# Kernel optimization log

Hardware: AMD Instinct MI355X
Metric: run time of the kernel (lower is better)

Reference implementation:

```python
import jax, jax.numpy as jnp
import numpy as np

N = 50000       # nodes
E = 800000      # edges (before self-loops)
B = 1024        # graphs
D = 256         # emb = hidden = representation size
OUT = 128
NFEAT = 9       # OGB atom features
VOCAB = 100
NLAYERS = 4     # 1 + hidden_layers(2) + 1
NEG_SLOPE = 0.2


def setup_inputs() -> dict:
    key = jax.random.key(0)
    ks = jax.random.split(key, 10)
    x = jax.random.randint(ks[0], (N, NFEAT), 0, VOCAB)
    edge_index = jax.random.randint(ks[1], (2, E), 0, N)
    batch = jnp.sort(jax.random.randint(ks[2], (N,), 0, B))
    atom_emb = jax.random.normal(ks[3], (NFEAT, VOCAB, D), jnp.float32) * 0.1
    Ws = jax.random.normal(ks[4], (NLAYERS, D, D), jnp.float32) * (1.0 / np.sqrt(D))
    a_src = jax.random.normal(ks[5], (NLAYERS, D), jnp.float32) * 0.1
    a_dst = jax.random.normal(ks[6], (NLAYERS, D), jnp.float32) * 0.1
    biases = jnp.zeros((NLAYERS, D), jnp.float32)
    lin_w = jax.random.normal(ks[7], (3 * D, OUT), jnp.float32) * (1.0 / np.sqrt(3 * D))
    lin_b = jnp.zeros((OUT,), jnp.float32)
    return dict(x=x, edge_index=edge_index, batch=batch, atom_emb=atom_emb,
                Ws=Ws, a_src=a_src, a_dst=a_dst, biases=biases,
                lin_w=lin_w, lin_b=lin_b)


def _gat_layer(h, src, dst, W, asrc, adst, b):
    # PyG GATConv, heads=1: linear transform, per-edge additive attention,
    # segment softmax over incoming edges of each target, scatter-add aggregate.
    h = h @ W                                        # [N, D]
    s = jnp.einsum('nd,d->n', h, asrc)               # source-side score
    t = jnp.einsum('nd,d->n', h, adst)               # target-side score
    e = jax.nn.leaky_relu(s[src] + t[dst], NEG_SLOPE)  # [E']
    m = jax.ops.segment_max(e, dst, num_segments=N)  # segment softmax (stable)
    e = jnp.exp(e - m[dst])
    denom = jax.ops.segment_sum(e, dst, num_segments=N)
    alpha = e / denom[dst]                           # self-loops ensure denom > 0
    out = jax.ops.segment_sum(alpha[:, None] * h[src], dst, num_segments=N)
    return out + b


def reference(x, edge_index, batch, atom_emb, Ws, a_src, a_dst, biases, lin_w, lin_b):
    # AtomEncoder: sum of per-feature embedding lookups -> [N, D]
    h = atom_emb[jnp.arange(NFEAT)[:, None], x.T].sum(axis=0)
    # add self-loops once (GATConv default add_self_loops=True)
    loops = jnp.arange(N)
    src = jnp.concatenate([edge_index[0], loops])
    dst = jnp.concatenate([edge_index[1], loops])
    for l in range(NLAYERS):
        h = _gat_layer(h, src, dst, Ws[l], a_src[l], a_dst[l], biases[l])
        h = jax.nn.relu(h)
    # global mean / add / max pooling over graphs
    count = jax.ops.segment_sum(jnp.ones((N,), h.dtype), batch, num_segments=B)
    x_add = jax.ops.segment_sum(h, batch, num_segments=B)
    x_mean = x_add / jnp.maximum(count, 1.0)[:, None]
    x_max = jax.ops.segment_max(h, batch, num_segments=B)
    x_max = jnp.where(count[:, None] > 0, x_max, 0.0)
    feats = jnp.concatenate([x_mean, x_add, x_max], axis=1)  # [B, 3D]
    # dropout is identity in eval mode
    return feats @ lin_w + lin_b
```

## Files before the change

### kernel.cpp

```cpp
#include <hip/hip_runtime.h>
#include <math.h>

#define N_NODES 50000
#define N_EDGES 800000
#define NGRAPH  1024
#define D       256
#define OUTD    128
#define NFEAT   9
#define VOCABSZ 100
#define NLAYERS 4
#define NEG_SLOPE 0.2f
#define SCAN_NBLK ((N_NODES + 255) / 256)

typedef __attribute__((ext_vector_type(8))) short short8;
typedef __attribute__((ext_vector_type(4))) float f32x4;

static __device__ __forceinline__ unsigned short f2bf(float f) {
    unsigned int u = __float_as_uint(f);
    u = (u + 0x7FFFu + ((u >> 16) & 1u)) >> 16;
    return (unsigned short)u;
}
static __device__ __forceinline__ float bf2f(unsigned short u) {
    return __uint_as_float(((unsigned int)u) << 16);
}

#define GLOAD_LDS16(g, l) __builtin_amdgcn_global_load_lds( \
    (const __attribute__((address_space(1))) void*)(g), \
    (__attribute__((address_space(3))) void*)(l), 16, 0, 0)

__global__ void set_deg_one(int* deg) {
    int v = blockIdx.x * blockDim.x + threadIdx.x;
    if (v < N_NODES) deg[v] = 1;
}

__global__ void hist_dst(const int* __restrict__ dst, int* __restrict__ deg) {
    int e = blockIdx.x * blockDim.x + threadIdx.x;
    if (e < N_EDGES) atomicAdd(&deg[dst[e]], 1);
}

__global__ __launch_bounds__(256) void block_sum(const int* __restrict__ deg, int* __restrict__ bsum) {
    int i = blockIdx.x * 256 + threadIdx.x;
    int v = (i < N_NODES) ? deg[i] : 0;
    #pragma unroll
    for (int off = 32; off; off >>= 1) v += __shfl_down(v, off, 64);
    __shared__ int ws[4];
    if ((threadIdx.x & 63) == 0) ws[threadIdx.x >> 6] = v;
    __syncthreads();
    if (threadIdx.x == 0) bsum[blockIdx.x] = ws[0] + ws[1] + ws[2] + ws[3];
}

__global__ __launch_bounds__(256) void scan_bsum(int* __restrict__ bsum, int* __restrict__ rowptr) {
    __shared__ int sh[256];
    int tid = threadIdx.x;
    int v = (tid < SCAN_NBLK) ? bsum[tid] : 0;
    sh[tid] = v;
    __syncthreads();
    for (int off = 1; off < 256; off <<= 1) {
        int u = (tid >= off) ? sh[tid - off] : 0;
        __syncthreads();
        sh[tid] += u;
        __syncthreads();
    }
    if (tid < SCAN_NBLK) bsum[tid] = (tid > 0) ? sh[tid - 1] : 0;
    if (tid == SCAN_NBLK - 1) rowptr[N_NODES] = sh[tid];
}

__global__ __launch_bounds__(256) void scan_block(const int* __restrict__ deg,
                                                  const int* __restrict__ boffs,
                                                  int* __restrict__ rowptr) {
    __shared__ int sh[256];
    int tid = threadIdx.x;
    int i = blockIdx.x * 256 + tid;
    int v = (i < N_NODES) ? deg[i] : 0;
    sh[tid] = v;
    __syncthreads();
    for (int off = 1; off < 256; off <<= 1) {
        int u = (tid >= off) ? sh[tid - off] : 0;
        __syncthreads();
        sh[tid] += u;
        __syncthreads();
    }
    if (i < N_NODES) rowptr[i] = boffs[blockIdx.x] + sh[tid] - v;
}

__global__ void init_cursor(const int* __restrict__ rowptr, int* __restrict__ cursor, int* __restrict__ ssrc) {
    int v = blockIdx.x * blockDim.x + threadIdx.x;
    if (v < N_NODES) {
        int p = rowptr[v];
        cursor[v] = p + 1;
        ssrc[p] = v;
    }
}

__global__ void scatter_edges(const int* __restrict__ src, const int* __restrict__ dst,
                              int* __restrict__ cursor, int* __restrict__ ssrc) {
    int e = blockIdx.x * blockDim.x + threadIdx.x;
    if (e < N_EDGES) {
        int pos = atomicAdd(&cursor[dst[e]], 1);
        ssrc[pos] = src[e];
    }
}

__global__ __launch_bounds__(256) void wt_kernel(const float* __restrict__ W, unsigned short* __restrict__ Wt) {
    int t = blockIdx.x * 256 + threadIdx.x;
    int l = t >> 16;
    int k = (t >> 8) & 255;
    int n = t & 255;
    float v = W[t];
    Wt[(l << 16) + n * 256 + k] = f2bf(v);
}

__global__ void zero_st(float* __restrict__ s, float* __restrict__ t) {
    int i = blockIdx.x * blockDim.x + threadIdx.x;
    if (i < N_NODES) { s[i] = 0.f; t[i] = 0.f; }
}

__global__ __launch_bounds__(256) void atom_encoder(const int* __restrict__ x,
                                                    const float* __restrict__ emb,
                                                    unsigned short* __restrict__ h) {
    int node = blockIdx.x * 4 + (threadIdx.x >> 6);
    int lane = threadIdx.x & 63;
    if (node >= N_NODES) return;
    float4 acc = make_float4(0.f, 0.f, 0.f, 0.f);
    #pragma unroll
    for (int f = 0; f < NFEAT; ++f) {
        int xi = x[node * NFEAT + f];
        float4 v = *(const float4*)&emb[(size_t)(f * VOCABSZ + xi) * D + lane * 4];
        acc.x += v.x; acc.y += v.y; acc.z += v.z; acc.w += v.w;
    }
    ushort4 o;
    o.x = f2bf(acc.x); o.y = f2bf(acc.y); o.z = f2bf(acc.z); o.w = f2bf(acc.w);
    *(ushort4*)&h[node * D + lane * 4] = o;
}

#define GBM 128
#define GBN 128
#define GBK 64
__global__ __launch_bounds__(256) void gemm_bf16(const unsigned short* __restrict__ A,
                                                 const unsigned short* __restrict__ Wt,
                                                 const float* __restrict__ asrc,
                                                 const float* __restrict__ adst,
                                                 unsigned short* __restrict__ C,
                                                 float* __restrict__ s_out,
                                                 float* __restrict__ t_out) {
    __shared__ unsigned short a_s[2][GBM * GBK];
    __shared__ unsigned short b_s[2][GBM * GBK];
    int row0 = blockIdx.x * GBM;
    int col0 = blockIdx.y * GBN;
    int tid = threadIdx.x;
    int wid = tid >> 6;
    int lane = tid & 63;
    int wm = wid >> 1, wn = wid & 1;
    int l15 = lane & 15;
    int lhi = lane >> 4;

    int srcA[4], srcB[4];
    #pragma unroll
    for (int q = 0; q < 4; ++q) {
        int slot = (wid * 4 + q) * 64 + lane;
        int r = slot >> 3, c = slot & 7;
        int ra = row0 + r; if (ra > N_NODES - 1) ra = N_NODES - 1;
        srcA[q] = ra * D + ((c ^ (r & 7)) << 3);
        srcB[q] = (col0 + r) * D + ((c ^ (r & 7)) << 3);
    }

    f32x4 acc[4][4];
    #pragma unroll
    for (int i = 0; i < 4; ++i)
        #pragma unroll
        for (int j = 0; j < 4; ++j) acc[i][j] = (f32x4){0.f, 0.f, 0.f, 0.f};

    #pragma unroll
    for (int q = 0; q < 4; ++q) {
        GLOAD_LDS16(A + srcA[q], &a_s[0][(wid * 4 + q) * 512]);
        GLOAD_LDS16(Wt + srcB[q], &b_s[0][(wid * 4 + q) * 512]);
    }
    __syncthreads();

    #pragma unroll
    for (int step = 0; step < 4; ++step) {
        int cur = step & 1;
        if (step < 3) {
            int k0 = (step + 1) * GBK;
            #pragma unroll
            for (int q = 0; q < 4; ++q) {
                GLOAD_LDS16(A + srcA[q] + k0, &a_s[cur ^ 1][(wid * 4 + q) * 512]);
                GLOAD_LDS16(Wt + srcB[q] + k0, &b_s[cur ^ 1][(wid * 4 + q) * 512]);
            }
        }
        #pragma unroll
        for (int ks = 0; ks < 2; ++ks) {
            short8 af[4], bf[4];
            #pragma unroll
            for (int m = 0; m < 4; ++m) {
                int r = wm * 64 + m * 16 + l15;
                int c = ks * 4 + lhi;
                af[m] = *(const short8*)&a_s[cur][r * GBK + ((c ^ (r & 7)) << 3)];
            }
            #pragma unroll
            for (int n = 0; n < 4; ++n) {
                int r = wn * 64 + n * 16 + l15;
                int c = ks * 4 + lhi;
                bf[n] = *(const short8*)&b_s[cur][r * GBK + ((c ^ (r & 7)) << 3)];
            }
            #pragma unroll
            for (int m = 0; m < 4; ++m)
                #pragma unroll
                for (int n = 0; n < 4; ++n)
                    acc[m][n] = __builtin_amdgcn_mfma_f32_16x16x32_bf16(af[m], bf[n], acc[m][n], 0, 0, 0);
        }
        __syncthreads();
    }

    #pragma unroll
    for (int m = 0; m < 4; ++m) {
        #pragma unroll
        for (int r = 0; r < 4; ++r) {
            int grow = row0 + wm * 64 + m * 16 + lhi * 4 + r;
            if (grow < N_NODES) {
                #pragma unroll
                for (int n = 0; n < 4; ++n) {
                    int gcol = col0 + wn * 64 + n * 16 + l15;
                    C[(size_t)grow * D + gcol] = f2bf(acc[m][n][r]);
                }
            }
        }
    }

    float av[4], bv[4];
    #pragma unroll
    for (int n = 0; n < 4; ++n) {
        int gcol = col0 + wn * 64 + n * 16 + l15;
        av[n] = asrc[gcol];
        bv[n] = adst[gcol];
    }
    #pragma unroll
    for (int m = 0; m < 4; ++m) {
        #pragma unroll
        for (int r = 0; r < 4; ++r) {
            float ps = 0.f, pt = 0.f;
            #pragma unroll
            for (int n = 0; n < 4; ++n) {
                ps += acc[m][n][r] * av[n];
                pt += acc[m][n][r] * bv[n];
            }
            #pragma unroll
            for (int off = 1; off < 16; off <<= 1) {
                ps += __shfl_xor(ps, off, 64);
                pt += __shfl_xor(pt, off, 64);
            }
            int grow = row0 + wm * 64 + m * 16 + lhi * 4 + r;
            if (l15 == 0 && grow < N_NODES) {
                atomicAdd(&s_out[grow], ps);
                atomicAdd(&t_out[grow], pt);
            }
        }
    }
}

__global__ __launch_bounds__(256) void aggregate_kernel(const unsigned short* __restrict__ hW,
                                                        const float* __restrict__ s,
                                                        const float* __restrict__ t,
                                                        const int* __restrict__ rowptr,
                                                        const int* __restrict__ ssrc,
                                                        const float* __restrict__ bias,
                                                        unsigned short* __restrict__ hout) {
    int v = (blockIdx.x * blockDim.x + threadIdx.x) >> 6;
    int lane = threadIdx.x & 63;
    if (v >= N_NODES) return;
    int beg = rowptr[v];
    int deg = rowptr[v + 1] - beg;
    float tv = t[v];
    float m = -1e30f;
    float denom = 0.f;
    float acc[8];
    #pragma unroll
    for (int j = 0; j < 8; ++j) acc[j] = 0.f;
    int half = lane >> 5;
    int l32 = lane & 31;

    for (int base = 0; base < deg; base += 64) {
        int rem = deg - base; if (rem > 64) rem = 64;
        int u = 0; float e = -1e30f;
        if (lane < rem) {
            u = ssrc[beg + base + lane];
            float ev = s[u] + tv;
            e = (ev > 0.f) ? ev : NEG_SLOPE * ev;
        }
        float cm = e;
        #pragma unroll
        for (int off = 32; off; off >>= 1) cm = fmaxf(cm, __shfl_xor(cm, off, 64));
        float newm = fmaxf(m, cm);
        float scale = __expf(m - newm);
        float p = (lane < rem) ? __expf(e - newm) : 0.f;
        float ws = p;
        #pragma unroll
        for (int off = 32; off; off >>= 1) ws += __shfl_xor(ws, off, 64);
        denom = denom * scale + ws;
        m = newm;
        #pragma unroll
        for (int j = 0; j < 8; ++j) acc[j] *= scale;
        for (int i = 0; i < rem; i += 4) {
            int idx0 = i + half;
            int idx1 = i + 2 + half;
            float p0 = __shfl(p, idx0, 64);
            int   u0 = __shfl(u, idx0, 64);
            float p1 = __shfl(p, idx1, 64);
            int   u1 = __shfl(u, idx1, 64);
            short8 hv0 = *(const short8*)&hW[(size_t)u0 * D + l32 * 8];
            short8 hv1 = *(const short8*)&hW[(size_t)u1 * D + l32 * 8];
            #pragma unroll
            for (int j = 0; j < 8; ++j)
                acc[j] += p0 * bf2f((unsigned short)hv0[j]);
            #pragma unroll
            for (int j = 0; j < 8; ++j)
                acc[j] += p1 * bf2f((unsigned short)hv1[j]);
        }
    }
    #pragma unroll
    for (int j = 0; j < 8; ++j) acc[j] += __shfl_xor(acc[j], 32, 64);
    float inv = 1.f / denom;
    if (half == 0) {
        float4 b0 = *(const float4*)&bias[l32 * 8];
        float4 b1 = *(const float4*)&bias[l32 * 8 + 4];
        float bb[8] = {b0.x, b0.y, b0.z, b0.w, b1.x, b1.y, b1.z, b1.w};
        short8 o;
        #pragma unroll
        for (int j = 0; j < 8; ++j) {
            float val = fmaxf(acc[j] * inv + bb[j], 0.f);
            o[j] = (short)f2bf(val);
        }
        *(short8*)&hout[(size_t)v * D + l32 * 8] = o;
    }
}

__global__ void growptr_kernel(const int* __restrict__ batch, int* __restrict__ growptr) {
    int n = blockIdx.x * blockDim.x + threadIdx.x;
    if (n >= N_NODES) return;
    int b = batch[n];
    int prev = (n == 0) ? -1 : batch[n - 1];
    for (int g = prev + 1; g <= b; ++g) growptr[g] = n;
    if (n == N_NODES - 1) {
        for (int g = b + 1; g <= NGRAPH; ++g) growptr[g] = N_NODES;
    }
}

__global__ __launch_bounds__(256) void pool_kernel(const unsigned short* __restrict__ h,
                                                   const int* __restrict__ growptr,
                                                   float* __restrict__ feats) {
    int g = (blockIdx.x * blockDim.x + threadIdx.x) >> 6;
    int lane = threadIdx.x & 63;
    if (g >= NGRAPH) return;
    int beg = growptr[g], end = growptr[g + 1];
    float4 add = make_float4(0.f, 0.f, 0.f, 0.f);
    float4 mx = make_float4(-1e30f, -1e30f, -1e30f, -1e30f);
    for (int v = beg; v < end; ++v) {
        ushort4 hv = *(const ushort4*)&h[(size_t)v * D + lane * 4];
        float h0 = bf2f(hv.x), h1 = bf2f(hv.y), h2 = bf2f(hv.z), h3 = bf2f(hv.w);
        add.x += h0; add.y += h1; add.z += h2; add.w += h3;
        mx.x = fmaxf(mx.x, h0); mx.y = fmaxf(mx.y, h1);
        mx.z = fmaxf(mx.z, h2); mx.w = fmaxf(mx.w, h3);
    }
    float cnt = (float)(end - beg);
    float invc = 1.f / fmaxf(cnt, 1.f);
    if (cnt <= 0.f) { mx = make_float4(0.f, 0.f, 0.f, 0.f); }
    float4 mean = make_float4(add.x * invc, add.y * invc, add.z * invc, add.w * invc);
    float* fr = feats + (size_t)g * 3 * D;
    *(float4*)&fr[0 * D + 4 * lane] = mean;
    *(float4*)&fr[1 * D + 4 * lane] = add;
    *(float4*)&fr[2 * D + 4 * lane] = mx;
}

__global__ __launch_bounds__(128) void final_linear(const float* __restrict__ feats,
                                                    const float* __restrict__ lw,
                                                    const float* __restrict__ lb,
                                                    float* __restrict__ out) {
    int g = blockIdx.x;
    int j = threadIdx.x;
    __shared__ float f[3 * D];
    for (int i = j; i < 3 * D; i += OUTD) f[i] = feats[(size_t)g * 3 * D + i];
    __syncthreads();
    float acc = lb[j];
    #pragma unroll 8
    for (int k = 0; k < 3 * D; ++k)
        acc += f[k] * lw[k * OUTD + j];
    out[g * OUTD + j] = acc;
}

extern "C" void kernel_launch(void* const* d_in, const int* in_sizes, int n_in,
                              void* d_out, int out_size, void* d_ws, size_t ws_size,
                              hipStream_t stream) {
    const int*   x        = (const int*)d_in[0];
    const int*   edge_idx = (const int*)d_in[1];
    const int*   batch    = (const int*)d_in[2];
    const float* atom_emb = (const float*)d_in[3];
    const float* Ws       = (const float*)d_in[4];
    const float* a_src    = (const float*)d_in[5];
    const float* a_dst    = (const float*)d_in[6];
    const float* biases   = (const float*)d_in[7];
    const float* lin_w    = (const float*)d_in[8];
    const float* lin_b    = (const float*)d_in[9];
    float* out = (float*)d_out;

    char* ws = (char*)d_ws;
    size_t off = 0;
    auto alloc = [&](size_t bytes) -> void* {
        void* p = ws + off;
        off += (bytes + 255) & ~(size_t)255;
        return p;
    };
    unsigned short* bufA = (unsigned short*)alloc(sizeof(short) * (size_t)N_NODES * D);
    unsigned short* bufB = (unsigned short*)alloc(sizeof(short) * (size_t)N_NODES * D);
    unsigned short* Wt   = (unsigned short*)alloc(sizeof(short) * NLAYERS * D * D);
    float* s      = (float*)alloc(sizeof(float) * N_NODES);
    float* t      = (float*)alloc(sizeof(float) * N_NODES);
    int*   deg    = (int*)alloc(sizeof(int) * N_NODES);
    int*   rowptr = (int*)alloc(sizeof(int) * (N_NODES + 1));
    int*   bsum   = (int*)alloc(sizeof(int) * 256);
    int*   ssrc   = (int*)alloc(sizeof(int) * (N_EDGES + N_NODES));
    int*   growp  = (int*)alloc(sizeof(int) * (NGRAPH + 1));
    float* feats  = (float*)alloc(sizeof(float) * (size_t)NGRAPH * 3 * D);

    const int* esrc = edge_idx;
    const int* edst = edge_idx + N_EDGES;

    set_deg_one<<<(N_NODES + 255) / 256, 256, 0, stream>>>(deg);
    hist_dst<<<(N_EDGES + 255) / 256, 256, 0, stream>>>(edst, deg);
    block_sum<<<SCAN_NBLK, 256, 0, stream>>>(deg, bsum);
    scan_bsum<<<1, 256, 0, stream>>>(bsum, rowptr);
    scan_block<<<SCAN_NBLK, 256, 0, stream>>>(deg, bsum, rowptr);
    init_cursor<<<(N_NODES + 255) / 256, 256, 0, stream>>>(rowptr, deg, ssrc);
    scatter_edges<<<(N_EDGES + 255) / 256, 256, 0, stream>>>(esrc, edst, deg, ssrc);

    wt_kernel<<<NLAYERS * D * D / 256, 256, 0, stream>>>(Ws, Wt);
    atom_encoder<<<(N_NODES + 3) / 4, 256, 0, stream>>>(x, atom_emb, bufA);

    for (int l = 0; l < NLAYERS; ++l) {
        zero_st<<<(N_NODES + 255) / 256, 256, 0, stream>>>(s, t);
        dim3 ggrid((N_NODES + GBM - 1) / GBM, D / GBN);
        gemm_bf16<<<ggrid, 256, 0, stream>>>(bufA, Wt + (size_t)l * D * D,
                                             a_src + l * D, a_dst + l * D,
                                             bufB, s, t);
        aggregate_kernel<<<(N_NODES + 3) / 4, 256, 0, stream>>>(bufB, s, t, rowptr, ssrc,
                                                                biases + l * D, bufA);
    }

    growptr_kernel<<<(N_NODES + 255) / 256, 256, 0, stream>>>(batch, growp);
    pool_kernel<<<(NGRAPH + 3) / 4, 256, 0, stream>>>(bufA, growp, feats);
    final_linear<<<NGRAPH, OUTD, 0, stream>>>(feats, lin_w, lin_b, out);
}
```

Measured before the change: 536.2 us.

## Unroll aggregate gathers with packed FMA, unroll pooling, batch graphs in final linear

The aggregation loop now issues four neighbour row gathers per iteration instead of two and accumulates with packed two-wide float math using bit-shift bf16 unpacking. Pooling unrolls the node loop by four to raise memory-level parallelism. The final linear layer processes eight graphs per block, so each weight load is reused eight times. Costs are higher register pressure in aggregate and fewer blocks in the final linear.

```diff
diff --git a/kernel.cpp b/kernel.cpp
--- a/kernel.cpp
+++ b/kernel.cpp
@@ -14,6 +14,7 @@
 
 typedef __attribute__((ext_vector_type(8))) short short8;
 typedef __attribute__((ext_vector_type(4))) float f32x4;
+typedef __attribute__((ext_vector_type(2))) float f32x2;
 
 static __device__ __forceinline__ unsigned short f2bf(float f) {
     unsigned int u = __float_as_uint(f);
@@ -273,11 +274,12 @@
     float tv = t[v];
     float m = -1e30f;
     float denom = 0.f;
-    float acc[8];
-    #pragma unroll
-    for (int j = 0; j < 8; ++j) acc[j] = 0.f;
+    f32x2 acc2[4];
+    #pragma unroll
+    for (int j = 0; j < 4; ++j) acc2[j] = (f32x2){0.f, 0.f};
     int half = lane >> 5;
     int l32 = lane & 31;
+    const unsigned short* hbase = hW + (size_t)l32 * 8;
 
     for (int base = 0; base < deg; base += 64) {
         int rem = deg - base; if (rem > 64) rem = 64;
@@ -299,35 +301,55 @@
         denom = denom * scale + ws;
         m = newm;
         #pragma unroll
-        for (int j = 0; j < 8; ++j) acc[j] *= scale;
-        for (int i = 0; i < rem; i += 4) {
-            int idx0 = i + half;
-            int idx1 = i + 2 + half;
-            float p0 = __shfl(p, idx0, 64);
-            int   u0 = __shfl(u, idx0, 64);
-            float p1 = __shfl(p, idx1, 64);
-            int   u1 = __shfl(u, idx1, 64);
-            short8 hv0 = *(const short8*)&hW[(size_t)u0 * D + l32 * 8];
-            short8 hv1 = *(const short8*)&hW[(size_t)u1 * D + l32 * 8];
-            #pragma unroll
-            for (int j = 0; j < 8; ++j)
-                acc[j] += p0 * bf2f((unsigned short)hv0[j]);
-            #pragma unroll
-            for (int j = 0; j < 8; ++j)
-                acc[j] += p1 * bf2f((unsigned short)hv1[j]);
-        }
-    }
-    #pragma unroll
-    for (int j = 0; j < 8; ++j) acc[j] += __shfl_xor(acc[j], 32, 64);
+        for (int j = 0; j < 4; ++j) acc2[j] *= scale;
+        for (int i = 0; i < rem; i += 8) {
+            float pj[4]; int uj[4];
+            #pragma unroll
+            for (int j = 0; j < 4; ++j) {
+                int idx = i + 2 * j + half;
+                pj[j] = __shfl(p, idx, 64);
+                uj[j] = __shfl(u, idx, 64);
+            }
+            uint4 w[4];
+            #pragma unroll
+            for (int j = 0; j < 4; ++j)
+                w[j] = *(const uint4*)(hbase + ((size_t)uj[j] << 8));
+            #pragma unroll
+            for (int j = 0; j < 4; ++j) {
+                f32x2 p2 = (f32x2){pj[j], pj[j]};
+                unsigned int ww;
+                f32x2 h2;
+                ww = w[j].x;
+                h2 = (f32x2){__uint_as_float(ww << 16), __uint_as_float(ww & 0xffff0000u)};
+                acc2[0] += p2 * h2;
+                ww = w[j].y;
+                h2 = (f32x2){__uint_as_float(ww << 16), __uint_as_float(ww & 0xffff0000u)};
+                acc2[1] += p2 * h2;
+                ww = w[j].z;
+                h2 = (f32x2){__uint_as_float(ww << 16), __uint_as_float(ww & 0xffff0000u)};
+                acc2[2] += p2 * h2;
+                ww = w[j].w;
+                h2 = (f32x2){__uint_as_float(ww << 16), __uint_as_float(ww & 0xffff0000u)};
+                acc2[3] += p2 * h2;
+            }
+        }
+    }
+    #pragma unroll
+    for (int j = 0; j < 4; ++j) {
+        acc2[j].x += __shfl_xor(acc2[j].x, 32, 64);
+        acc2[j].y += __shfl_xor(acc2[j].y, 32, 64);
+    }
     float inv = 1.f / denom;
     if (half == 0) {
         float4 b0 = *(const float4*)&bias[l32 * 8];
         float4 b1 = *(const float4*)&bias[l32 * 8 + 4];
         float bb[8] = {b0.x, b0.y, b0.z, b0.w, b1.x, b1.y, b1.z, b1.w};
+        float av[8] = {acc2[0].x, acc2[0].y, acc2[1].x, acc2[1].y,
+                       acc2[2].x, acc2[2].y, acc2[3].x, acc2[3].y};
         short8 o;
         #pragma unroll
         for (int j = 0; j < 8; ++j) {
-            float val = fmaxf(acc[j] * inv + bb[j], 0.f);
+            float val = fmaxf(av[j] * inv + bb[j], 0.f);
             o[j] = (short)f2bf(val);
         }
         *(short8*)&hout[(size_t)v * D + l32 * 8] = o;
@@ -354,12 +376,27 @@
     int beg = growptr[g], end = growptr[g + 1];
     float4 add = make_float4(0.f, 0.f, 0.f, 0.f);
     float4 mx = make_float4(-1e30f, -1e30f, -1e30f, -1e30f);
-    for (int v = beg; v < end; ++v) {
+    int v = beg;
+    for (; v + 4 <= end; v += 4) {
+        ushort4 h0 = *(const ushort4*)&h[(size_t)(v + 0) * D + lane * 4];
+        ushort4 h1 = *(const ushort4*)&h[(size_t)(v + 1) * D + lane * 4];
+        ushort4 h2 = *(const ushort4*)&h[(size_t)(v + 2) * D + lane * 4];
+        ushort4 h3 = *(const ushort4*)&h[(size_t)(v + 3) * D + lane * 4];
+        ushort4 hs[4] = {h0, h1, h2, h3};
+        #pragma unroll
+        for (int q = 0; q < 4; ++q) {
+            float a0 = bf2f(hs[q].x), a1 = bf2f(hs[q].y), a2 = bf2f(hs[q].z), a3 = bf2f(hs[q].w);
+            add.x += a0; add.y += a1; add.z += a2; add.w += a3;
+            mx.x = fmaxf(mx.x, a0); mx.y = fmaxf(mx.y, a1);
+            mx.z = fmaxf(mx.z, a2); mx.w = fmaxf(mx.w, a3);
+        }
+    }
+    for (; v < end; ++v) {
         ushort4 hv = *(const ushort4*)&h[(size_t)v * D + lane * 4];
-        float h0 = bf2f(hv.x), h1 = bf2f(hv.y), h2 = bf2f(hv.z), h3 = bf2f(hv.w);
-        add.x += h0; add.y += h1; add.z += h2; add.w += h3;
-        mx.x = fmaxf(mx.x, h0); mx.y = fmaxf(mx.y, h1);
-        mx.z = fmaxf(mx.z, h2); mx.w = fmaxf(mx.w, h3);
+        float a0 = bf2f(hv.x), a1 = bf2f(hv.y), a2 = bf2f(hv.z), a3 = bf2f(hv.w);
+        add.x += a0; add.y += a1; add.z += a2; add.w += a3;
+        mx.x = fmaxf(mx.x, a0); mx.y = fmaxf(mx.y, a1);
+        mx.z = fmaxf(mx.z, a2); mx.w = fmaxf(mx.w, a3);
     }
     float cnt = (float)(end - beg);
     float invc = 1.f / fmaxf(cnt, 1.f);
@@ -371,20 +408,30 @@
     *(float4*)&fr[2 * D + 4 * lane] = mx;
 }
 
+#define GPB 8
 __global__ __launch_bounds__(128) void final_linear(const float* __restrict__ feats,
                                                     const float* __restrict__ lw,
                                                     const float* __restrict__ lb,
                                                     float* __restrict__ out) {
-    int g = blockIdx.x;
+    int g0 = blockIdx.x * GPB;
     int j = threadIdx.x;
-    __shared__ float f[3 * D];
-    for (int i = j; i < 3 * D; i += OUTD) f[i] = feats[(size_t)g * 3 * D + i];
+    __shared__ float f[GPB][3 * D];
+    for (int i = j; i < GPB * 3 * D; i += OUTD)
+        f[i / (3 * D)][i % (3 * D)] = feats[(size_t)g0 * 3 * D + i];
     __syncthreads();
-    float acc = lb[j];
-    #pragma unroll 8
-    for (int k = 0; k < 3 * D; ++k)
-        acc += f[k] * lw[k * OUTD + j];
-    out[g * OUTD + j] = acc;
+    float acc[GPB];
+    float lbv = lb[j];
+    #pragma unroll
+    for (int g = 0; g < GPB; ++g) acc[g] = lbv;
+    for (int k = 0; k < 3 * D; ++k) {
+        float w = lw[k * OUTD + j];
+        #pragma unroll
+        for (int g = 0; g < GPB; ++g)
+            acc[g] += f[g][k] * w;
+    }
+    #pragma unroll
+    for (int g = 0; g < GPB; ++g)
+        out[(g0 + g) * OUTD + j] = acc[g];
 }
 
 extern "C" void kernel_launch(void* const* d_in, const int* in_sizes, int n_in,
@@ -447,5 +494,5 @@
 
     growptr_kernel<<<(N_NODES + 255) / 256, 256, 0, stream>>>(batch, growp);
     pool_kernel<<<(NGRAPH + 3) / 4, 256, 0, stream>>>(bufA, growp, feats);
-    final_linear<<<NGRAPH, OUTD, 0, stream>>>(feats, lin_w, lin_b, out);
-}
+    final_linear<<<NGRAPH / GPB, OUTD, 0, stream>>>(feats, lin_w, lin_b, out);
+}
```

Result: no change. 537.2 us (+0.2%).

## Stage GEMM output through LDS, batch final linear, hoist s/t zeroing, unroll pooling

Applied to the files above, without the earlier changes.

Four separate changes. The GEMM epilogue now writes the bf16 tile to padded shared memory and then issues coalesced 16-byte row stores, replacing scattered 2-byte stores. The per-layer zero_st launches become one up-front init over per-layer s/t buffers. The final linear processes 8 graphs per block so each weight load is reused. Pooling is unrolled by 4 nodes. The cost is extra LDS traffic and a barrier in the epilogue, plus a little more workspace for the per-layer s/t buffers.

```diff
diff --git a/kernel.cpp b/kernel.cpp
--- a/kernel.cpp
+++ b/kernel.cpp
@@ -28,9 +28,10 @@
     (const __attribute__((address_space(1))) void*)(g), \
     (__attribute__((address_space(3))) void*)(l), 16, 0, 0)
 
-__global__ void set_deg_one(int* deg) {
-    int v = blockIdx.x * blockDim.x + threadIdx.x;
-    if (v < N_NODES) deg[v] = 1;
+__global__ void init_all(int* __restrict__ deg, float* __restrict__ s_all, float* __restrict__ t_all) {
+    int i = blockIdx.x * blockDim.x + threadIdx.x;
+    if (i < N_NODES) deg[i] = 1;
+    if (i < NLAYERS * N_NODES) { s_all[i] = 0.f; t_all[i] = 0.f; }
 }
 
 __global__ void hist_dst(const int* __restrict__ dst, int* __restrict__ deg) {
@@ -108,11 +109,6 @@
     int n = t & 255;
     float v = W[t];
     Wt[(l << 16) + n * 256 + k] = f2bf(v);
-}
-
-__global__ void zero_st(float* __restrict__ s, float* __restrict__ t) {
-    int i = blockIdx.x * blockDim.x + threadIdx.x;
-    if (i < N_NODES) { s[i] = 0.f; t[i] = 0.f; }
 }
 
 __global__ __launch_bounds__(256) void atom_encoder(const int* __restrict__ x,
@@ -143,8 +139,7 @@
                                                  unsigned short* __restrict__ C,
                                                  float* __restrict__ s_out,
                                                  float* __restrict__ t_out) {
-    __shared__ unsigned short a_s[2][GBM * GBK];
-    __shared__ unsigned short b_s[2][GBM * GBK];
+    __shared__ unsigned short smem[32768];
     int row0 = blockIdx.x * GBM;
     int col0 = blockIdx.y * GBN;
     int tid = threadIdx.x;
@@ -172,8 +167,8 @@
 
     #pragma unroll
     for (int q = 0; q < 4; ++q) {
-        GLOAD_LDS16(A + srcA[q], &a_s[0][(wid * 4 + q) * 512]);
-        GLOAD_LDS16(Wt + srcB[q], &b_s[0][(wid * 4 + q) * 512]);
+        GLOAD_LDS16(A + srcA[q], &smem[(wid * 4 + q) * 512]);
+        GLOAD_LDS16(Wt + srcB[q], &smem[16384 + (wid * 4 + q) * 512]);
     }
     __syncthreads();
 
@@ -184,10 +179,12 @@
             int k0 = (step + 1) * GBK;
             #pragma unroll
             for (int q = 0; q < 4; ++q) {
-                GLOAD_LDS16(A + srcA[q] + k0, &a_s[cur ^ 1][(wid * 4 + q) * 512]);
-                GLOAD_LDS16(Wt + srcB[q] + k0, &b_s[cur ^ 1][(wid * 4 + q) * 512]);
-            }
-        }
+                GLOAD_LDS16(A + srcA[q] + k0, &smem[(cur ^ 1) * 8192 + (wid * 4 + q) * 512]);
+                GLOAD_LDS16(Wt + srcB[q] + k0, &smem[16384 + (cur ^ 1) * 8192 + (wid * 4 + q) * 512]);
+            }
+        }
+        const unsigned short* aS = &smem[cur * 8192];
+        const unsigned short* bS = &smem[16384 + cur * 8192];
         #pragma unroll
         for (int ks = 0; ks < 2; ++ks) {
             short8 af[4], bf[4];
@@ -195,13 +192,13 @@
             for (int m = 0; m < 4; ++m) {
                 int r = wm * 64 + m * 16 + l15;
                 int c = ks * 4 + lhi;
-                af[m] = *(const short8*)&a_s[cur][r * GBK + ((c ^ (r & 7)) << 3)];
+                af[m] = *(const short8*)&aS[r * GBK + ((c ^ (r & 7)) << 3)];
             }
             #pragma unroll
             for (int n = 0; n < 4; ++n) {
                 int r = wn * 64 + n * 16 + l15;
                 int c = ks * 4 + lhi;
-                bf[n] = *(const short8*)&b_s[cur][r * GBK + ((c ^ (r & 7)) << 3)];
+                bf[n] = *(const short8*)&bS[r * GBK + ((c ^ (r & 7)) << 3)];
             }
             #pragma unroll
             for (int m = 0; m < 4; ++m)
@@ -212,18 +209,29 @@
         __syncthreads();
     }
 
+    unsigned short* c_s = smem;
     #pragma unroll
     for (int m = 0; m < 4; ++m) {
         #pragma unroll
         for (int r = 0; r < 4; ++r) {
-            int grow = row0 + wm * 64 + m * 16 + lhi * 4 + r;
-            if (grow < N_NODES) {
-                #pragma unroll
-                for (int n = 0; n < 4; ++n) {
-                    int gcol = col0 + wn * 64 + n * 16 + l15;
-                    C[(size_t)grow * D + gcol] = f2bf(acc[m][n][r]);
-                }
-            }
+            int lr = wm * 64 + m * 16 + lhi * 4 + r;
+            #pragma unroll
+            for (int n = 0; n < 4; ++n) {
+                int lc = wn * 64 + n * 16 + l15;
+                c_s[lr * 132 + lc] = f2bf(acc[m][n][r]);
+            }
+        }
+    }
+    __syncthreads();
+    #pragma unroll
+    for (int p = 0; p < 8; ++p) {
+        int slot = p * 256 + tid;
+        int r2 = slot >> 4;
+        int c2 = slot & 15;
+        int grow = row0 + r2;
+        if (grow < N_NODES) {
+            short8 vv = *(const short8*)&c_s[r2 * 132 + c2 * 8];
+            *(short8*)&C[(size_t)grow * D + col0 + c2 * 8] = vv;
         }
     }
 
@@ -354,12 +362,27 @@
     int beg = growptr[g], end = growptr[g + 1];
     float4 add = make_float4(0.f, 0.f, 0.f, 0.f);
     float4 mx = make_float4(-1e30f, -1e30f, -1e30f, -1e30f);
-    for (int v = beg; v < end; ++v) {
+    int v = beg;
+    for (; v + 4 <= end; v += 4) {
+        ushort4 h0 = *(const ushort4*)&h[(size_t)(v + 0) * D + lane * 4];
+        ushort4 h1 = *(const ushort4*)&h[(size_t)(v + 1) * D + lane * 4];
+        ushort4 h2 = *(const ushort4*)&h[(size_t)(v + 2) * D + lane * 4];
+        ushort4 h3 = *(const ushort4*)&h[(size_t)(v + 3) * D + lane * 4];
+        ushort4 hs[4] = {h0, h1, h2, h3};
+        #pragma unroll
+        for (int q = 0; q < 4; ++q) {
+            float a0 = bf2f(hs[q].x), a1 = bf2f(hs[q].y), a2 = bf2f(hs[q].z), a3 = bf2f(hs[q].w);
+            add.x += a0; add.y += a1; add.z += a2; add.w += a3;
+            mx.x = fmaxf(mx.x, a0); mx.y = fmaxf(mx.y, a1);
+            mx.z = fmaxf(mx.z, a2); mx.w = fmaxf(mx.w, a3);
+        }
+    }
+    for (; v < end; ++v) {
         ushort4 hv = *(const ushort4*)&h[(size_t)v * D + lane * 4];
-        float h0 = bf2f(hv.x), h1 = bf2f(hv.y), h2 = bf2f(hv.z), h3 = bf2f(hv.w);
-        add.x += h0; add.y += h1; add.z += h2; add.w += h3;
-        mx.x = fmaxf(mx.x, h0); mx.y = fmaxf(mx.y, h1);
-        mx.z = fmaxf(mx.z, h2); mx.w = fmaxf(mx.w, h3);
+        float a0 = bf2f(hv.x), a1 = bf2f(hv.y), a2 = bf2f(hv.z), a3 = bf2f(hv.w);
+        add.x += a0; add.y += a1; add.z += a2; add.w += a3;
+        mx.x = fmaxf(mx.x, a0); mx.y = fmaxf(mx.y, a1);
+        mx.z = fmaxf(mx.z, a2); mx.w = fmaxf(mx.w, a3);
     }
     float cnt = (float)(end - beg);
     float invc = 1.f / fmaxf(cnt, 1.f);
@@ -371,20 +394,30 @@
     *(float4*)&fr[2 * D + 4 * lane] = mx;
 }
 
+#define GPB 8
 __global__ __launch_bounds__(128) void final_linear(const float* __restrict__ feats,
                                                     const float* __restrict__ lw,
                                                     const float* __restrict__ lb,
                                                     float* __restrict__ out) {
-    int g = blockIdx.x;
+    int g0 = blockIdx.x * GPB;
     int j = threadIdx.x;
-    __shared__ float f[3 * D];
-    for (int i = j; i < 3 * D; i += OUTD) f[i] = feats[(size_t)g * 3 * D + i];
-    __syncthreads();
-    float acc = lb[j];
-    #pragma unroll 8
-    for (int k = 0; k < 3 * D; ++k)
-        acc += f[k] * lw[k * OUTD + j];
-    out[g * OUTD + j] = acc;
+    __shared__ float f[GPB][3 * D];
+    for (int i = j; i < GPB * 3 * D; i += OUTD)
+        f[i / (3 * D)][i % (3 * D)] = feats[(size_t)g0 * 3 * D + i];
+    __syncthreads();
+    float acc[GPB];
+    float lbv = lb[j];
+    #pragma unroll
+    for (int g = 0; g < GPB; ++g) acc[g] = lbv;
+    for (int k = 0; k < 3 * D; ++k) {
+        float w = lw[k * OUTD + j];
+        #pragma unroll
+        for (int g = 0; g < GPB; ++g)
+            acc[g] += f[g][k] * w;
+    }
+    #pragma unroll
+    for (int g = 0; g < GPB; ++g)
+        out[(g0 + g) * OUTD + j] = acc[g];
 }
 
 extern "C" void kernel_launch(void* const* d_in, const int* in_sizes, int n_in,
@@ -409,11 +442,11 @@
         off += (bytes + 255) & ~(size_t)255;
         return p;
     };
-    unsigned short* bufA = (unsigned short*)alloc(sizeof(short) * (size_t)N_NODES * D);
-    unsigned short* bufB = (unsigned short*)alloc(sizeof(short) * (size_t)N_NODES * D);
-    unsigned short* Wt   = (unsigned short*)alloc(sizeof(short) * NLAYERS * D * D);
-    float* s      = (float*)alloc(sizeof(float) * N_NODES);
-    float* t      = (float*)alloc(sizeof(float) * N_NODES);
+    unsigned short* bufA  = (unsigned short*)alloc(sizeof(short) * (size_t)N_NODES * D);
+    unsigned short* bufB  = (unsigned short*)alloc(sizeof(short) * (size_t)N_NODES * D);
+    unsigned short* Wt    = (unsigned short*)alloc(sizeof(short) * NLAYERS * D * D);
+    float* s_all  = (float*)alloc(sizeof(float) * NLAYERS * N_NODES);
+    float* t_all  = (float*)alloc(sizeof(float) * NLAYERS * N_NODES);
     int*   deg    = (int*)alloc(sizeof(int) * N_NODES);
     int*   rowptr = (int*)alloc(sizeof(int) * (N_NODES + 1));
     int*   bsum   = (int*)alloc(sizeof(int) * 256);
@@ -424,7 +457,7 @@
     const int* esrc = edge_idx;
     const int* edst = edge_idx + N_EDGES;
 
-    set_deg_one<<<(N_NODES + 255) / 256, 256, 0, stream>>>(deg);
+    init_all<<<(NLAYERS * N_NODES + 255) / 256, 256, 0, stream>>>(deg, s_all, t_all);
     hist_dst<<<(N_EDGES + 255) / 256, 256, 0, stream>>>(edst, deg);
     block_sum<<<SCAN_NBLK, 256, 0, stream>>>(deg, bsum);
     scan_bsum<<<1, 256, 0, stream>>>(bsum, rowptr);
@@ -436,16 +469,18 @@
     atom_encoder<<<(N_NODES + 3) / 4, 256, 0, stream>>>(x, atom_emb, bufA);
 
     for (int l = 0; l < NLAYERS; ++l) {
-        zero_st<<<(N_NODES + 255) / 256, 256, 0, stream>>>(s, t);
         dim3 ggrid((N_NODES + GBM - 1) / GBM, D / GBN);
         gemm_bf16<<<ggrid, 256, 0, stream>>>(bufA, Wt + (size_t)l * D * D,
                                              a_src + l * D, a_dst + l * D,
-                                             bufB, s, t);
-        aggregate_kernel<<<(N_NODES + 3) / 4, 256, 0, stream>>>(bufB, s, t, rowptr, ssrc,
-                                                                biases + l * D, bufA);
+                                             bufB, s_all + (size_t)l * N_NODES,
+                                             t_all + (size_t)l * N_NODES);
+        aggregate_kernel<<<(N_NODES + 3) / 4, 256, 0, stream>>>(bufB,
+                                             s_all + (size_t)l * N_NODES,
+                                             t_all + (size_t)l * N_NODES,
+                                             rowptr, ssrc, biases + l * D, bufA);
     }
 
     growptr_kernel<<<(N_NODES + 255) / 256, 256, 0, stream>>>(batch, growp);
     pool_kernel<<<(NGRAPH + 3) / 4, 256, 0, stream>>>(bufA, growp, feats);
-    final_linear<<<NGRAPH, OUTD, 0, stream>>>(feats, lin_w, lin_b, out);
-}
+    final_linear<<<NGRAPH / GPB, OUTD, 0, stream>>>(feats, lin_w, lin_b, out);
+}
```

Measured after the change: 529.6 us. About the same (-1.2%).
